# Kernel tuning notes

Measured on AMD Instinct MI355X. Metric: run time of the kernel, lower is better.

The kernel has to match this reference:

```python
import jax, jax.numpy as jnp
import numpy as np

B, L, CIN, H, K = 32, 4096, 128, 256, 3


def setup_inputs() -> dict:
    key = jax.random.key(0)
    k1, k2, k3 = jax.random.split(key, 3)
    x = jax.random.normal(k1, (B, L, CIN), dtype=jnp.float32)
    # Conv1d weight: (out_ch=3H, in_ch=CIN, kernel=K), fan-in scaled like torch default
    W = jax.random.normal(k2, (3 * H, CIN, K), dtype=jnp.float32) * (1.0 / np.sqrt(CIN * K))
    b = jax.random.normal(k3, (3 * H,), dtype=jnp.float32) * 0.01
    return {"x": x, "W": W, "b": b}


def reference(x, W, b):
    # x: (B, L, CIN) -> (B, CIN, L), matching torch's x.transpose(1, 2)
    xc = jnp.transpose(x, (0, 2, 1))
    # valid 1D conv -> (B, 3H, T) with T = L - K + 1
    conv = jax.lax.conv_general_dilated(
        xc, W, window_strides=(1,), padding="VALID",
        dimension_numbers=("NCH", "OIH", "NCH"),
    ) + b[None, :, None]
    Z, F, O = jnp.split(conv, 3, axis=1)
    Z = jnp.tanh(Z)
    F = jax.nn.sigmoid(F)
    O = jax.nn.sigmoid(O)
    # sequential fo-pool: h_t = O_t * (F_t * h_{t-1} + (1 - F_t) * Z_t)
    zs = jnp.moveaxis(Z, 2, 0)   # (T, B, H)
    fs = jnp.moveaxis(F, 2, 0)
    os_ = jnp.moveaxis(O, 2, 0)
    h0 = jnp.zeros((x.shape[0], H), dtype=Z.dtype)

    def step(h, zfo):
        z, f, o = zfo
        h = o * (f * h + (1.0 - f) * z)
        return h, None

    hT, _ = jax.lax.scan(step, h0, (zs, fs, os_))
    return hT  # (B, H): final hidden state
```

## Files before the change

kernel.cpp:

```cpp
#include <hip/hip_runtime.h>
#include <math.h>

#define B_    32
#define L_    4096
#define CIN_  128
#define H_    256
#define T_    4094
#define KTOT_ 384

#define MT_   128
#define NG_   192
#define NKT_  12
#define NCH_  512
#define NSEG_ 16
#define GP_   196

typedef float f32x4 __attribute__((ext_vector_type(4)));
typedef short s16x8 __attribute__((ext_vector_type(8)));

static __device__ __forceinline__ unsigned short f2bf(float f) {
  unsigned u = __builtin_bit_cast(unsigned, f);
  u = (u + 0x7FFFu + ((u >> 16) & 1u)) >> 16;
  return (unsigned short)u;
}

__global__ __launch_bounds__(256) void packW_bf16(const float* __restrict__ W,
                                                  unsigned short* __restrict__ Wb) {
  const int idx = blockIdx.x * 256 + threadIdx.x;
  const int e = idx & 7;
  int t = idx >> 3;
  const int c = t % NG_;
  t /= NG_;
  const int kgrp = t & 3;
  t >>= 2;
  const int kt = t % NKT_;
  const int g = t / NKT_;
  const int kk = kt * 32 + kgrp * 8 + e;
  const int i = kk & 127, k = kk >> 7;
  const int gate = c >> 6, hl = c & 63;
  const int oc = gate * 256 + g * 64 + hl;
  Wb[idx] = f2bf(W[(size_t)oc * KTOT_ + i * 3 + k]);
}

__global__ __launch_bounds__(512, 4) void conv_scan_mfma(
    const float* __restrict__ x, const unsigned short* __restrict__ Wb,
    const float* __restrict__ bias, float* __restrict__ Pws,
    float* __restrict__ Sws) {
  __shared__ __align__(16) char smem[64 * GP_ * 4];
  char* xs = smem;
  float* gs = (float*)smem;

  const int tid = threadIdx.x;
  const int w = tid >> 6;
  const int wm = w >> 2;
  const int wn = w & 3;
  const int l = tid & 63;
  const int lr = l & 15;
  const int lg = l >> 4;
  const int tb = blockIdx.x;
  const int g = blockIdx.y;
  const int bb = tb & 31;
  const int tblk = tb >> 5;
  const int t0 = tblk * MT_;

  for (int v = tid; v < 130 * 32; v += 512) {
    const int row = v >> 5;
    const int colb = (v & 31) * 8;
    int r = t0 + row;
    if (r > L_ - 1) r = L_ - 1;
    const float4 xv = *(const float4*)&x[((size_t)bb * L_ + r) * CIN_ + (v & 31) * 4];
    unsigned p0, p1;
    asm("v_cvt_pk_bf16_f32 %0, %1, %2" : "=v"(p0) : "v"(xv.x), "v"(xv.y));
    asm("v_cvt_pk_bf16_f32 %0, %1, %2" : "=v"(p1) : "v"(xv.z), "v"(xv.w));
    *(uint2*)(xs + row * 256 + (colb ^ ((row & 7) << 4))) = make_uint2(p0, p1);
  }

  const unsigned short* bp = Wb + (size_t)g * (NKT_ * 6144) + lg * 1536 + (wn * 48 + lr) * 8;

  f32x4 acc[4][3];
#pragma unroll
  for (int mi = 0; mi < 4; ++mi)
#pragma unroll
    for (int nj = 0; nj < 3; ++nj) acc[mi][nj] = (f32x4)0.f;

  __syncthreads();

#pragma unroll
  for (int kt = 0; kt < NKT_; ++kt) {
    const int kof = kt >> 2;
    const int cb = (kt & 3) * 64 + lg * 16;
    s16x8 b[3], a[4];
#pragma unroll
    for (int nj = 0; nj < 3; ++nj)
      b[nj] = *(const s16x8*)(bp + kt * 6144 + nj * 128);
#pragma unroll
    for (int mi = 0; mi < 4; ++mi) {
      const int row = wm * 64 + mi * 16 + lr + kof;
      a[mi] = *(const s16x8*)(xs + row * 256 + (cb ^ ((row & 7) << 4)));
    }
#pragma unroll
    for (int mi = 0; mi < 4; ++mi)
#pragma unroll
      for (int nj = 0; nj < 3; ++nj)
        acc[mi][nj] = __builtin_amdgcn_mfma_f32_16x16x32_bf16(a[mi], b[nj], acc[mi][nj], 0, 0, 0);
  }

  const float bz = bias[g * 64 + l];
  const float bf = bias[256 + g * 64 + l];
  const float bo = bias[512 + g * 64 + l];

#pragma unroll
  for (int p = 0; p < 2; ++p) {
    __syncthreads();
    if (wm == p) {
#pragma unroll
      for (int mi = 0; mi < 4; ++mi)
#pragma unroll
        for (int nj = 0; nj < 3; ++nj)
#pragma unroll
          for (int r = 0; r < 4; ++r) {
            const int rl = mi * 16 + lg * 4 + r;
            gs[rl * GP_ + wn * 48 + nj * 16 + lr] = acc[mi][nj][r];
          }
    }
    __syncthreads();
    float P = 1.f, S = 0.f;
#pragma unroll
    for (int mt = 0; mt < 8; ++mt) {
      const int t = t0 + p * 64 + w * 8 + mt;
      if (t < T_) {
        const int rl = w * 8 + mt;
        const float zr = gs[rl * GP_ + l] + bz;
        const float fr = gs[rl * GP_ + 64 + l] + bf;
        const float orr = gs[rl * GP_ + 128 + l] + bo;
        const float zc = fminf(fmaxf(zr, -15.f), 15.f);
        const float e2 = __expf(2.f * zc);
        const float zt = (e2 - 1.f) * __builtin_amdgcn_rcpf(e2 + 1.f);
        const float ft = __builtin_amdgcn_rcpf(1.f + __expf(-fr));
        const float ot = __builtin_amdgcn_rcpf(1.f + __expf(-orr));
        const float A = ot * ft;
        const float Bv = ot * (1.f - ft) * zt;
        S = A * S + Bv;
        P = A * P;
      }
    }
    const int c = tblk * 16 + p * 8 + w;
    const size_t o = ((size_t)bb * NCH_ + c) * H_ + g * 64 + l;
    Pws[o] = P;
    Sws[o] = S;
  }
}

__global__ __launch_bounds__(256) void combine1(const float* __restrict__ Pws,
                                                const float* __restrict__ Sws,
                                                float* __restrict__ P2,
                                                float* __restrict__ S2) {
  const int idx = blockIdx.x * 256 + threadIdx.x;
  const int b = idx >> 12;
  const int s = (idx >> 8) & 15;
  const int h = idx & 255;
  float P = 1.f, S = 0.f;
#pragma unroll 4
  for (int c = 0; c < 32; ++c) {
    const size_t o = ((size_t)b * NCH_ + s * 32 + c) * H_ + h;
    const float p = Pws[o];
    const float sv = Sws[o];
    S = p * S + sv;
    P = p * P;
  }
  P2[(b * NSEG_ + s) * H_ + h] = P;
  S2[(b * NSEG_ + s) * H_ + h] = S;
}

__global__ __launch_bounds__(256) void combine2(const float* __restrict__ P2,
                                                const float* __restrict__ S2,
                                                float* __restrict__ out) {
  const int idx = blockIdx.x * 256 + threadIdx.x;
  const int b = idx >> 8;
  const int h = idx & 255;
  float hv = 0.f;
#pragma unroll
  for (int s = 0; s < NSEG_; ++s) {
    const float p = P2[(b * NSEG_ + s) * H_ + h];
    const float sv = S2[(b * NSEG_ + s) * H_ + h];
    hv = p * hv + sv;
  }
  out[idx] = hv;
}

extern "C" void kernel_launch(void* const* d_in, const int* in_sizes, int n_in,
                              void* d_out, int out_size, void* d_ws, size_t ws_size,
                              hipStream_t stream) {
  const float* x = (const float*)d_in[0];
  const float* W = (const float*)d_in[1];
  const float* bias = (const float*)d_in[2];
  float* out = (float*)d_out;

  char* ws = (char*)d_ws;
  unsigned short* Wb = (unsigned short*)ws;
  float* Pws = (float*)(ws + (1 << 20));
  float* Sws = (float*)(ws + 17 * (1 << 20));
  float* P2  = (float*)(ws + 33 * (1 << 20));
  float* S2  = (float*)(ws + 33 * (1 << 20) + (512 << 10));

  packW_bf16<<<1152, 256, 0, stream>>>(W, Wb);
  conv_scan_mfma<<<dim3(1024, 4), 512, 0, stream>>>(x, Wb, bias, Pws, Sws);
  combine1<<<512, 256, 0, stream>>>(Pws, Sws, P2, S2);
  combine2<<<32, 256, 0, stream>>>(P2, S2, out);
}
```

Before: 207.2 us.

## Fuse chunk combine into conv kernel and shrink gate staging buffer

Each conv block now combines its 32 per-wave chunk (P,S) pairs in shared memory and writes a single pair per block. This removes the 16MB-per-array workspace writes and the combine1 kernel launch, leaving one small final combine. The gate staging buffer is halved by processing four 32-row passes instead of two 64-row passes, and launch bounds are raised to ask for 6 blocks per SM. The extra passes add barriers, and the serial combine runs on one wave while the other waves idle.

Measured after the change: 252.2 us. 1.22x slower.

```diff
diff --git a/kernel.cpp b/kernel.cpp
--- a/kernel.cpp
+++ b/kernel.cpp
@@ -9,10 +9,9 @@
 #define KTOT_ 384
 
 #define MT_   128
+#define NTB_  32
 #define NG_   192
 #define NKT_  12
-#define NCH_  512
-#define NSEG_ 16
 #define GP_   196
 
 typedef float f32x4 __attribute__((ext_vector_type(4)));
@@ -42,13 +41,14 @@
   Wb[idx] = f2bf(W[(size_t)oc * KTOT_ + i * 3 + k]);
 }
 
-__global__ __launch_bounds__(512, 4) void conv_scan_mfma(
+__global__ __launch_bounds__(512, 6) void conv_scan_mfma(
     const float* __restrict__ x, const unsigned short* __restrict__ Wb,
-    const float* __restrict__ bias, float* __restrict__ Pws,
-    float* __restrict__ Sws) {
-  __shared__ __align__(16) char smem[64 * GP_ * 4];
+    const float* __restrict__ bias, float* __restrict__ Pc,
+    float* __restrict__ Sc) {
+  __shared__ __align__(16) char smem[25088 + 16384];
   char* xs = smem;
   float* gs = (float*)smem;
+  float* pbuf = (float*)(smem + 25088);
 
   const int tid = threadIdx.x;
   const int w = tid >> 6;
@@ -110,26 +110,28 @@
   const float bo = bias[512 + g * 64 + l];
 
 #pragma unroll
-  for (int p = 0; p < 2; ++p) {
+  for (int p = 0; p < 4; ++p) {
     __syncthreads();
-    if (wm == p) {
-#pragma unroll
-      for (int mi = 0; mi < 4; ++mi)
+    if (wm == (p >> 1)) {
+#pragma unroll
+      for (int mo = 0; mo < 2; ++mo) {
+        const int mi = 2 * (p & 1) + mo;
 #pragma unroll
         for (int nj = 0; nj < 3; ++nj)
 #pragma unroll
           for (int r = 0; r < 4; ++r) {
-            const int rl = mi * 16 + lg * 4 + r;
+            const int rl = mo * 16 + lg * 4 + r;
             gs[rl * GP_ + wn * 48 + nj * 16 + lr] = acc[mi][nj][r];
           }
+      }
     }
     __syncthreads();
     float P = 1.f, S = 0.f;
 #pragma unroll
-    for (int mt = 0; mt < 8; ++mt) {
-      const int t = t0 + p * 64 + w * 8 + mt;
+    for (int mt = 0; mt < 4; ++mt) {
+      const int t = t0 + p * 32 + w * 4 + mt;
       if (t < T_) {
-        const int rl = w * 8 + mt;
+        const int rl = w * 4 + mt;
         const float zr = gs[rl * GP_ + l] + bz;
         const float fr = gs[rl * GP_ + 64 + l] + bf;
         const float orr = gs[rl * GP_ + 128 + l] + bo;
@@ -144,46 +146,39 @@
         P = A * P;
       }
     }
-    const int c = tblk * 16 + p * 8 + w;
-    const size_t o = ((size_t)bb * NCH_ + c) * H_ + g * 64 + l;
-    Pws[o] = P;
-    Sws[o] = S;
-  }
-}
-
-__global__ __launch_bounds__(256) void combine1(const float* __restrict__ Pws,
-                                                const float* __restrict__ Sws,
-                                                float* __restrict__ P2,
-                                                float* __restrict__ S2) {
-  const int idx = blockIdx.x * 256 + threadIdx.x;
-  const int b = idx >> 12;
-  const int s = (idx >> 8) & 15;
-  const int h = idx & 255;
-  float P = 1.f, S = 0.f;
-#pragma unroll 4
-  for (int c = 0; c < 32; ++c) {
-    const size_t o = ((size_t)b * NCH_ + s * 32 + c) * H_ + h;
-    const float p = Pws[o];
-    const float sv = Sws[o];
-    S = p * S + sv;
-    P = p * P;
-  }
-  P2[(b * NSEG_ + s) * H_ + h] = P;
-  S2[(b * NSEG_ + s) * H_ + h] = S;
-}
-
-__global__ __launch_bounds__(256) void combine2(const float* __restrict__ P2,
-                                                const float* __restrict__ S2,
-                                                float* __restrict__ out) {
+    const int ci = p * 8 + w;
+    pbuf[ci * 128 + 2 * l] = P;
+    pbuf[ci * 128 + 2 * l + 1] = S;
+  }
+
+  __syncthreads();
+  if (w == 0) {
+    float P = 1.f, S = 0.f;
+#pragma unroll 8
+    for (int ci = 0; ci < 32; ++ci) {
+      const float pp = pbuf[ci * 128 + 2 * l];
+      const float ss = pbuf[ci * 128 + 2 * l + 1];
+      S = pp * S + ss;
+      P = pp * P;
+    }
+    const size_t o = ((size_t)bb * NTB_ + tblk) * H_ + g * 64 + l;
+    Pc[o] = P;
+    Sc[o] = S;
+  }
+}
+
+__global__ __launch_bounds__(256) void combine_kernel(const float* __restrict__ Pc,
+                                                      const float* __restrict__ Sc,
+                                                      float* __restrict__ out) {
   const int idx = blockIdx.x * 256 + threadIdx.x;
   const int b = idx >> 8;
   const int h = idx & 255;
   float hv = 0.f;
-#pragma unroll
-  for (int s = 0; s < NSEG_; ++s) {
-    const float p = P2[(b * NSEG_ + s) * H_ + h];
-    const float sv = S2[(b * NSEG_ + s) * H_ + h];
-    hv = p * hv + sv;
+#pragma unroll 8
+  for (int c = 0; c < NTB_; ++c) {
+    const float p = Pc[((size_t)b * NTB_ + c) * H_ + h];
+    const float s = Sc[((size_t)b * NTB_ + c) * H_ + h];
+    hv = p * hv + s;
   }
   out[idx] = hv;
 }
@@ -198,13 +193,10 @@
 
   char* ws = (char*)d_ws;
   unsigned short* Wb = (unsigned short*)ws;
-  float* Pws = (float*)(ws + (1 << 20));
-  float* Sws = (float*)(ws + 17 * (1 << 20));
-  float* P2  = (float*)(ws + 33 * (1 << 20));
-  float* S2  = (float*)(ws + 33 * (1 << 20) + (512 << 10));
+  float* Pc = (float*)(ws + (1 << 20));
+  float* Sc = (float*)(ws + 2 * (1 << 20));
 
   packW_bf16<<<1152, 256, 0, stream>>>(W, Wb);
-  conv_scan_mfma<<<dim3(1024, 4), 512, 0, stream>>>(x, Wb, bias, Pws, Sws);
-  combine1<<<512, 256, 0, stream>>>(Pws, Sws, P2, S2);
-  combine2<<<32, 256, 0, stream>>>(P2, S2, out);
-}
+  conv_scan_mfma<<<dim3(1024, 4), 512, 0, stream>>>(x, Wb, bias, Pc, Sc);
+  combine_kernel<<<32, 256, 0, stream>>>(Pc, Sc, out);
+}
```
